# Kernel optimization log

Hardware: AMD Instinct MI355X
Metric: run time of the kernel (lower is better)

Reference implementation:

```python
import jax, jax.numpy as jnp
import numpy as np

B, C, T = 32, 1536, 2048
BN = 128  # bottleneck channels


def setup_inputs() -> dict:
    key = jax.random.key(0)
    k1, k2, k3, k4, k5, k6 = jax.random.split(key, 6)
    x = jax.random.normal(k1, (B, C, T), dtype=jnp.float32)
    padding_mask = jax.random.randint(k2, (B, T), 0, 2) == 1
    W_tdnn = jax.random.normal(k3, (BN, C), dtype=jnp.float32) * (1.0 / np.sqrt(C))
    b_tdnn = jax.random.normal(k4, (BN,), dtype=jnp.float32) * 0.01
    W_attn = jax.random.normal(k5, (C, BN), dtype=jnp.float32) * (1.0 / np.sqrt(BN))
    b_attn = jax.random.normal(k6, (C,), dtype=jnp.float32) * 0.01
    return {"x": x, "padding_mask": padding_mask, "W_tdnn": W_tdnn,
            "b_tdnn": b_tdnn, "W_attn": W_attn, "b_attn": b_attn}


def reference(x, padding_mask, W_tdnn, b_tdnn, W_attn, b_attn):
    # pointwise conv1 (k=1) == channel-wise matmul: (B,C,T) -> (B,BN,T)
    e = jnp.tanh(jnp.einsum('oc,bct->bot', W_tdnn, x) + b_tdnn[None, :, None])
    # pointwise conv2: (B,BN,T) -> (B,C,T)
    a = jnp.einsum('co,bot->bct', W_attn, e) + b_attn[None, :, None]
    a = jnp.where(padding_mask[:, None, :], -1e9, a)
    alpha = jax.nn.softmax(a, axis=2)  # (B,C,T)
    mean = jnp.sum(alpha * x, axis=2)  # (B,C)
    var = jnp.sum(alpha * (x - mean[:, :, None]) ** 2, axis=2)
    std = jnp.sqrt(jnp.clip(var, 1e-9, None))
    return jnp.concatenate([mean, std], axis=1)  # (B,2C)
```

## Files before the change

### kernel.cpp

```cpp
#include <hip/hip_runtime.h>
#include <math.h>

#define Bn  32
#define Cn  1536
#define Tn  2048
#define BNn 128
#define SHIFT 12.0f

typedef __attribute__((ext_vector_type(8))) short bf16x8;
typedef __attribute__((ext_vector_type(4))) float fx4;

__device__ __forceinline__ unsigned int f2bf1(float f) {
    unsigned int u = __float_as_uint(f);
    return (u + 0x7fffu + ((u >> 16) & 1u)) >> 16;
}
__device__ __forceinline__ float fast_tanh(float v) {
    return 1.f - 2.f / (__expf(2.f * v) + 1.f);
}

__global__ void k_prep(const float* __restrict__ W1f, const float* __restrict__ Waf,
                       short* __restrict__ W1b, short* __restrict__ Wab) {
    int i = blockIdx.x * 256 + threadIdx.x;
    if (i < BNn * Cn) {
        W1b[i] = (short)f2bf1(W1f[i]);
        Wab[i] = (short)f2bf1(Waf[i]);
    }
}


#define P1_LOAD(XR, K0) do {                                                  \
    _Pragma("unroll") for (int p = 0; p < 2; ++p) {                           \
        const int c_ = cq + p * 32;                                           \
        _Pragma("unroll") for (int j = 0; j < 4; ++j)                         \
            XR[p][j] = *(const float4*)(xt + (size_t)((K0) + c_ + j) * Tn + t4); \
    }                                                                         \
} while (0)

#define P1_WRITE(XR) do {                                                     \
    _Pragma("unroll") for (int p = 0; p < 2; ++p) {                           \
        const int c_   = cq + p * 32;                                         \
        const int blk_ = c_ >> 3;                                             \
        const int sub_ = c_ & 7;                                              \
        _Pragma("unroll") for (int i2 = 0; i2 < 4; ++i2) {                    \
            const int t_ = t4 + i2;                                           \
            unsigned int lo_ = f2bf1(((const float*)&XR[p][0])[i2]) |         \
                               (f2bf1(((const float*)&XR[p][1])[i2]) << 16);  \
            unsigned int hi_ = f2bf1(((const float*)&XR[p][2])[i2]) |         \
                               (f2bf1(((const float*)&XR[p][3])[i2]) << 16);  \
            const int idx_ = t_ * 64 + ((blk_ ^ (t_ & 7)) << 3) + sub_;       \
            *(uint2*)(sA + idx_) = make_uint2(lo_, hi_);                      \
        }                                                                     \
    }                                                                         \
} while (0)

#define P1_COMPUTE(K0) do {                                                   \
    _Pragma("unroll") for (int kt = 0; kt < 2; ++kt) {                        \
        bf16x8 bq_[4];                                                        \
        _Pragma("unroll") for (int nn = 0; nn < 4; ++nn)                      \
            bq_[nn] = *(const bf16x8*)(W1 + (size_t)(wo + nn * 16 + ln) * Cn  \
                                       + (K0) + kt * 32 + g * 8);             \
        bf16x8 af_[4];                                                        \
        _Pragma("unroll") for (int mm = 0; mm < 4; ++mm) {                    \
            const int t_ = wt + mm * 16 + ln;                                 \
            af_[mm] = *(const bf16x8*)(sA + t_ * 64                           \
                                       + (((kt * 4 + g) ^ (t_ & 7)) << 3));   \
        }                                                                     \
        _Pragma("unroll") for (int mm = 0; mm < 4; ++mm)                      \
            _Pragma("unroll") for (int nn = 0; nn < 4; ++nn)                  \
                acc[mm][nn] = __builtin_amdgcn_mfma_f32_16x16x32_bf16(        \
                    af_[mm], bq_[nn], acc[mm][nn], 0, 0, 0);                  \
    }                                                                         \
} while (0)

#define P2_CR(I) (((Cn - 64) - ((I) >> 1) * 64) + wc + ((I) & 1) * 16 + ln)

#define P2_LOAD(BQ, XQ, I) do {                                               \
    const int cr_ = P2_CR(I);                                                 \
    _Pragma("unroll") for (int kt = 0; kt < 4; ++kt)                          \
        BQ[kt] = *(const bf16x8*)(Wab + (size_t)cr_ * BNn + kt * 32 + g * 8); \
    _Pragma("unroll") for (int mt = 0; mt < 4; ++mt)                          \
        XQ[mt] = *(const float4*)(xb + (size_t)cr_ * Tn                       \
                                  + t0g + wt + mt * 16 + g * 4);              \
} while (0)

#define P2_COMPUTE(BQ, XQ, I) do {                                           \
    fx4 a2_[4];                                                               \
    _Pragma("unroll") for (int mt = 0; mt < 4; ++mt)                          \
        a2_[mt] = (fx4){0.f, 0.f, 0.f, 0.f};                                  \
    _Pragma("unroll") for (int kt = 0; kt < 4; ++kt)                          \
        _Pragma("unroll") for (int mt = 0; mt < 4; ++mt)                      \
            a2_[mt] = __builtin_amdgcn_mfma_f32_16x16x32_bf16(                \
                af2[mt][kt], BQ[kt], a2_[mt], 0, 0, 0);                       \
    float s0_ = 0.f, s1_ = 0.f, s2_ = 0.f;                                    \
    _Pragma("unroll") for (int mt = 0; mt < 4; ++mt) {                        \
        _Pragma("unroll") for (int r = 0; r < 4; ++r) {                       \
            const int msk_ = ((const int*)&mv[mt])[r];                        \
            const float p_ = msk_ ? 0.f : __expf(a2_[mt][r] - SHIFT);         \
            const float xv_ = ((const float*)&XQ[mt])[r];                     \
            s0_ += p_; s1_ += p_ * xv_; s2_ += p_ * xv_ * xv_;                \
        }                                                                     \
    }                                                                         \
    s0_ += __shfl_xor(s0_, 16); s1_ += __shfl_xor(s1_, 16);                   \
    s2_ += __shfl_xor(s2_, 16);                                               \
    s0_ += __shfl_xor(s0_, 32); s1_ += __shfl_xor(s1_, 32);                   \
    s2_ += __shfl_xor(s2_, 32);                                               \
    if (g == 0) {                                                             \
        const int cr_ = P2_CR(I);                                             \
        *(float4*)&part[(((size_t)b * 32 + chunk) * Cn + cr_) * 4] =          \
            make_float4(s0_, s1_, s2_, 0.f);                                  \
    }                                                                         \
} while (0)

__global__ __launch_bounds__(256, 2) void k_fused(
    const float* __restrict__ x, const short* __restrict__ W1,
    const float* __restrict__ bias, const short* __restrict__ Wab,
    const int* __restrict__ mask, float* __restrict__ part)
{
    __shared__ short sA[128 * 64];
    __shared__ short sE[128 * 128];

    const int b    = blockIdx.y;
    const int t0g  = blockIdx.x * 128;
    const int tid  = threadIdx.x;
    const int lane = tid & 63;
    const int wv   = tid >> 6;
    const int ln   = lane & 15;
    const int g    = lane >> 4;
    const int wt   = (wv & 1) * 64;
    const int wo   = (wv >> 1) * 64;

    const float* xb = x + (size_t)b * Cn * Tn;
    const float* xt = xb + t0g;

    const int t4 = (tid & 31) * 4;
    const int cq = (tid >> 5) * 4;

    fx4 acc[4][4];
    #pragma unroll
    for (int i = 0; i < 4; ++i)
        #pragma unroll
        for (int j = 0; j < 4; ++j) acc[i][j] = (fx4){0.f, 0.f, 0.f, 0.f};

    float4 xrA[2][4], xrB[2][4];
    P1_LOAD(xrA, 0);
    for (int k0 = 0; k0 < Cn; k0 += 128) {
        __syncthreads();
        P1_WRITE(xrA);
        __syncthreads();
        P1_LOAD(xrB, k0 + 64);
        P1_COMPUTE(k0);
        __syncthreads();
        P1_WRITE(xrB);
        __syncthreads();
        if (k0 + 128 < Cn) P1_LOAD(xrA, k0 + 128);
        P1_COMPUTE(k0 + 64);
    }

    float bs[4];
    #pragma unroll
    for (int nn = 0; nn < 4; ++nn) bs[nn] = bias[wo + nn * 16 + ln];

    #pragma unroll
    for (int mm = 0; mm < 4; ++mm)
        #pragma unroll
        for (int nn = 0; nn < 4; ++nn) {
            #pragma unroll
            for (int r = 0; r < 4; ++r) {
                const int t = wt + mm * 16 + g * 4 + r;
                const int o = wo + nn * 16 + ln;
                const float v = fast_tanh(acc[mm][nn][r] + bs[nn]);
                sE[t * 128 + (((o >> 3) ^ (t & 15)) << 3) + (o & 7)] = (short)f2bf1(v);
            }
        }
    __syncthreads();

    bf16x8 af2[4][4];
    #pragma unroll
    for (int mt = 0; mt < 4; ++mt)
        #pragma unroll
        for (int kt = 0; kt < 4; ++kt) {
            const int t = wt + mt * 16 + ln;
            af2[mt][kt] = *(const bf16x8*)(sE + t * 128 + (((kt * 4 + g) ^ (t & 15)) << 3));
        }

    int4 mv[4];
    #pragma unroll
    for (int mt = 0; mt < 4; ++mt)
        mv[mt] = *(const int4*)(mask + (size_t)b * Tn + t0g + wt + mt * 16 + g * 4);

    const int wc    = (wv >> 1) * 32;
    const int chunk = blockIdx.x * 2 + (wv & 1);

    bf16x8 bA[4], bB[4];
    float4 xA[4], xB[4];
    P2_LOAD(bA, xA, 0);
    for (int i = 0; i < 48; i += 2) {
        P2_LOAD(bB, xB, i + 1);
        P2_COMPUTE(bA, xA, i);
        if (i + 2 < 48) P2_LOAD(bA, xA, i + 2);
        P2_COMPUTE(bB, xB, i + 1);
    }
}

__global__ void k_merge(const float* __restrict__ part, float* __restrict__ out) {
    const int i = blockIdx.x * 256 + threadIdx.x;
    if (i >= Bn * Cn) return;
    const int b = i / Cn, c = i - b * Cn;
    float s0 = 0.f, s1 = 0.f, s2 = 0.f;
    #pragma unroll 8
    for (int sp = 0; sp < 32; ++sp) {
        const float4 v = *(const float4*)&part[(((size_t)b * 32 + sp) * Cn + c) * 4];
        s0 += v.x; s1 += v.y; s2 += v.z;
    }
    const float mean = s1 / s0;
    const float var  = fmaxf(s2 / s0 - mean * mean, 1e-9f);
    out[(size_t)b * (2 * Cn) + c]      = mean;
    out[(size_t)b * (2 * Cn) + Cn + c] = sqrtf(var);
}

extern "C" void kernel_launch(void* const* d_in, const int* in_sizes, int n_in,
                              void* d_out, int out_size, void* d_ws, size_t ws_size,
                              hipStream_t stream) {
    const float* x      = (const float*)d_in[0];
    const int*   mask   = (const int*)d_in[1];
    const float* W_tdnn = (const float*)d_in[2];
    const float* b_tdnn = (const float*)d_in[3];
    const float* W_attn = (const float*)d_in[4];
    float* out = (float*)d_out;

    short* W1b  = (short*)d_ws;
    short* Wab  = W1b + (size_t)BNn * Cn;
    float* part = (float*)(Wab + (size_t)BNn * Cn);

    k_prep<<<dim3((BNn * Cn + 255) / 256), 256, 0, stream>>>(W_tdnn, W_attn, W1b, Wab);
    k_fused<<<dim3(Tn / 128, Bn), 256, 0, stream>>>(x, W1b, b_tdnn, Wab, mask, part);
    k_merge<<<dim3((Bn * Cn + 255) / 256), 256, 0, stream>>>(part, out);
}
```

Before: 620.8 us.

## Stage W1 tiles into LDS asynchronously and replace partial merge with atomics

```diff
diff --git a/kernel.cpp b/kernel.cpp
--- a/kernel.cpp
+++ b/kernel.cpp
@@ -19,11 +19,28 @@
 }
 
 __global__ void k_prep(const float* __restrict__ W1f, const float* __restrict__ Waf,
-                       short* __restrict__ W1b, short* __restrict__ Wab) {
+                       short* __restrict__ W1b, short* __restrict__ Wab,
+                       float* __restrict__ accp) {
     int i = blockIdx.x * 256 + threadIdx.x;
     if (i < BNn * Cn) {
         W1b[i] = (short)f2bf1(W1f[i]);
         Wab[i] = (short)f2bf1(Waf[i]);
+    }
+    if (i < Bn * Cn)
+        *(float4*)&accp[(size_t)i * 4] = make_float4(0.f, 0.f, 0.f, 0.f);
+}
+
+__device__ __forceinline__ void stage_w1(short* sW, const short* __restrict__ W1,
+                                         int tid, int k0) {
+    #pragma unroll
+    for (int j = 0; j < 4; ++j) {
+        const int o   = (tid >> 3) + j * 32;
+        const int blk = (tid & 7) ^ (o & 7);
+        __builtin_amdgcn_global_load_lds(
+            (const __attribute__((address_space(1))) unsigned int*)
+                (W1 + (size_t)o * Cn + k0 + blk * 8),
+            (__attribute__((address_space(3))) unsigned int*)(sW + tid * 8 + j * 2048),
+            16, 0, 0);
     }
 }
 
@@ -53,12 +70,14 @@
     }                                                                         \
 } while (0)
 
-#define P1_COMPUTE(K0) do {                                                   \
+#define P1_COMPUTE(SW) do {                                                   \
     _Pragma("unroll") for (int kt = 0; kt < 2; ++kt) {                        \
         bf16x8 bq_[4];                                                        \
-        _Pragma("unroll") for (int nn = 0; nn < 4; ++nn)                      \
-            bq_[nn] = *(const bf16x8*)(W1 + (size_t)(wo + nn * 16 + ln) * Cn  \
-                                       + (K0) + kt * 32 + g * 8);             \
+        _Pragma("unroll") for (int nn = 0; nn < 4; ++nn) {                    \
+            const int o_ = wo + nn * 16 + ln;                                 \
+            bq_[nn] = *(const bf16x8*)((SW) + o_ * 64                         \
+                                       + (((kt * 4 + g) ^ (o_ & 7)) << 3));   \
+        }                                                                     \
         bf16x8 af_[4];                                                        \
         _Pragma("unroll") for (int mm = 0; mm < 4; ++mm) {                    \
             const int t_ = wt + mm * 16 + ln;                                 \
@@ -105,16 +124,17 @@
     s0_ += __shfl_xor(s0_, 32); s1_ += __shfl_xor(s1_, 32);                   \
     s2_ += __shfl_xor(s2_, 32);                                               \
     if (g == 0) {                                                             \
-        const int cr_ = P2_CR(I);                                             \
-        *(float4*)&part[(((size_t)b * 32 + chunk) * Cn + cr_) * 4] =          \
-            make_float4(s0_, s1_, s2_, 0.f);                                  \
+        float* ap_ = accp + ((size_t)b * Cn + P2_CR(I)) * 4;                  \
+        atomicAdd(ap_ + 0, s0_);                                              \
+        atomicAdd(ap_ + 1, s1_);                                              \
+        atomicAdd(ap_ + 2, s2_);                                              \
     }                                                                         \
 } while (0)
 
 __global__ __launch_bounds__(256, 2) void k_fused(
     const float* __restrict__ x, const short* __restrict__ W1,
     const float* __restrict__ bias, const short* __restrict__ Wab,
-    const int* __restrict__ mask, float* __restrict__ part)
+    const int* __restrict__ mask, float* __restrict__ accp)
 {
     __shared__ short sA[128 * 64];
     __shared__ short sE[128 * 128];
@@ -135,26 +155,33 @@
     const int t4 = (tid & 31) * 4;
     const int cq = (tid >> 5) * 4;
 
+    short* const sW0 = sE;
+    short* const sW1 = sE + 8192;
+
     fx4 acc[4][4];
     #pragma unroll
     for (int i = 0; i < 4; ++i)
         #pragma unroll
         for (int j = 0; j < 4; ++j) acc[i][j] = (fx4){0.f, 0.f, 0.f, 0.f};
 
-    float4 xrA[2][4], xrB[2][4];
-    P1_LOAD(xrA, 0);
-    for (int k0 = 0; k0 < Cn; k0 += 128) {
+    float4 xr[2][4];
+    stage_w1(sW0, W1, tid, 0);
+    P1_LOAD(xr, 0);
+
+    for (int i = 0; i < Cn / 64; ++i) {
+        const int k0 = i * 64;
+        short* const sWc = (i & 1) ? sW1 : sW0;
+        short* const sWn = (i & 1) ? sW0 : sW1;
         __syncthreads();
-        P1_WRITE(xrA);
+        P1_WRITE(xr);
         __syncthreads();
-        P1_LOAD(xrB, k0 + 64);
-        P1_COMPUTE(k0);
-        __syncthreads();
-        P1_WRITE(xrB);
-        __syncthreads();
-        if (k0 + 128 < Cn) P1_LOAD(xrA, k0 + 128);
-        P1_COMPUTE(k0 + 64);
-    }
+        if (i + 1 < Cn / 64) {
+            stage_w1(sWn, W1, tid, k0 + 64);
+            P1_LOAD(xr, k0 + 64);
+        }
+        P1_COMPUTE(sWc);
+    }
+    __syncthreads();
 
     float bs[4];
     #pragma unroll
@@ -188,8 +215,7 @@
     for (int mt = 0; mt < 4; ++mt)
         mv[mt] = *(const int4*)(mask + (size_t)b * Tn + t0g + wt + mt * 16 + g * 4);
 
-    const int wc    = (wv >> 1) * 32;
-    const int chunk = blockIdx.x * 2 + (wv & 1);
+    const int wc = (wv >> 1) * 32;
 
     bf16x8 bA[4], bB[4];
     float4 xA[4], xB[4];
@@ -202,18 +228,13 @@
     }
 }
 
-__global__ void k_merge(const float* __restrict__ part, float* __restrict__ out) {
+__global__ void k_final(const float* __restrict__ accp, float* __restrict__ out) {
     const int i = blockIdx.x * 256 + threadIdx.x;
     if (i >= Bn * Cn) return;
     const int b = i / Cn, c = i - b * Cn;
-    float s0 = 0.f, s1 = 0.f, s2 = 0.f;
-    #pragma unroll 8
-    for (int sp = 0; sp < 32; ++sp) {
-        const float4 v = *(const float4*)&part[(((size_t)b * 32 + sp) * Cn + c) * 4];
-        s0 += v.x; s1 += v.y; s2 += v.z;
-    }
-    const float mean = s1 / s0;
-    const float var  = fmaxf(s2 / s0 - mean * mean, 1e-9f);
+    const float4 v = *(const float4*)&accp[(size_t)i * 4];
+    const float mean = v.y / v.x;
+    const float var  = fmaxf(v.z / v.x - mean * mean, 1e-9f);
     out[(size_t)b * (2 * Cn) + c]      = mean;
     out[(size_t)b * (2 * Cn) + Cn + c] = sqrtf(var);
 }
@@ -230,9 +251,9 @@
 
     short* W1b  = (short*)d_ws;
     short* Wab  = W1b + (size_t)BNn * Cn;
-    float* part = (float*)(Wab + (size_t)BNn * Cn);
-
-    k_prep<<<dim3((BNn * Cn + 255) / 256), 256, 0, stream>>>(W_tdnn, W_attn, W1b, Wab);
-    k_fused<<<dim3(Tn / 128, Bn), 256, 0, stream>>>(x, W1b, b_tdnn, Wab, mask, part);
-    k_merge<<<dim3((Bn * Cn + 255) / 256), 256, 0, stream>>>(part, out);
-}
+    float* accp = (float*)(Wab + (size_t)BNn * Cn);
+
+    k_prep<<<dim3((BNn * Cn + 255) / 256), 256, 0, stream>>>(W_tdnn, W_attn, W1b, Wab, accp);
+    k_fused<<<dim3(Tn / 128, Bn), 256, 0, stream>>>(x, W1b, b_tdnn, Wab, mask, accp);
+    k_final<<<dim3((Bn * Cn + 255) / 256), 256, 0, stream>>>(accp, out);
+}
```

After: 633.5 us. 1.02x slower.
